# Kernel optimization log

Measured on AMD Instinct MI355X. Metric: run time of the kernel, lower is better.

The kernel has to match this reference:

```python
import jax, jax.numpy as jnp
import numpy as np

N = 131072

def _project(feat, x, y):
    # bilinear sample: feat is [H, W, C], x/y are float pixel coords [N]
    x1 = jnp.floor(x); x2 = jnp.ceil(x)
    y1 = jnp.floor(y); y2 = jnp.ceil(y)
    xi1 = x1.astype(jnp.int32); xi2 = x2.astype(jnp.int32)
    yi1 = y1.astype(jnp.int32); yi2 = y2.astype(jnp.int32)
    # JAX clamps out-of-range gather indices (matches GPU tf.gather_nd edge behavior)
    Q11 = feat[xi1, yi1]
    Q12 = feat[xi1, yi2]
    Q21 = feat[xi2, yi1]
    Q22 = feat[xi2, yi2]
    w11 = ((x2 - x) * (y2 - y))[:, None]
    w21 = ((x - x1) * (y2 - y))[:, None]
    w12 = ((x2 - x) * (y - y1))[:, None]
    w22 = ((x - x1) * (y - y1))[:, None]
    return w11 * Q11 + w21 * Q21 + w12 * Q12 + w22 * Q22


def setup_inputs() -> dict:
    key = jax.random.key(0)
    k1, k2, k3, k4, k5 = jax.random.split(key, 5)
    coord = jax.random.normal(k1, (N, 3), dtype=jnp.float32)
    # ensure points are in front of the camera (Z < 0) as assumed by the projection
    coord = coord.at[:, 2].set(-jnp.abs(coord[:, 2]) - 1.0)
    feat1 = jax.random.normal(k2, (56, 56, 64), dtype=jnp.float32)
    feat2 = jax.random.normal(k3, (28, 28, 128), dtype=jnp.float32)
    feat3 = jax.random.normal(k4, (14, 14, 256), dtype=jnp.float32)
    feat4 = jax.random.normal(k5, (7, 7, 512), dtype=jnp.float32)
    return {"coord": coord, "feat1": feat1, "feat2": feat2, "feat3": feat3, "feat4": feat4}


def reference(coord, feat1, feat2, feat3, feat4):
    X = coord[:, 0]; Y = coord[:, 1]; Z = coord[:, 2]
    h = 248.0 * (-Y / -Z) + 112.0
    w = 248.0 * (X / -Z) + 112.0
    h = jnp.clip(h, 0.0, 223.0)
    w = jnp.clip(w, 0.0, 223.0)
    out1 = _project(feat1, h / (224.0 / 56), w / (224.0 / 56))
    out2 = _project(feat2, h / (224.0 / 28), w / (224.0 / 28))
    out3 = _project(feat3, h / (224.0 / 14), w / (224.0 / 14))
    out4 = _project(feat4, h / (224.0 / 7), w / (224.0 / 7))
    return jnp.concatenate([coord, out1, out2, out3, out4], axis=1)
```

## Files before the change

kernel.cpp:

```cpp
#include <hip/hip_runtime.h>


typedef float f4 __attribute__((ext_vector_type(4)));
typedef f4 uf4 __attribute__((aligned(4)));

struct BL {
    f4  wt;
    int b11, b21, b12, b22;
};

template <int C, int G>
__device__ __forceinline__ BL make_bl(float x, float y) {
    float x1 = floorf(x), x2 = ceilf(x);
    float y1 = floorf(y), y2 = ceilf(y);
    int xi1 = min((int)x1, G - 1), xi2 = min((int)x2, G - 1);
    int yi1 = min((int)y1, G - 1), yi2 = min((int)y2, G - 1);
    float wx2 = x2 - x, wx1 = x - x1;
    float wy2 = y2 - y, wy1 = y - y1;
    BL r;
    r.wt = (f4){wx2 * wy2, wx1 * wy2, wx2 * wy1, wx1 * wy1};
    const int W = C / 4;
    r.b11 = (xi1 * G + yi1) * W;
    r.b21 = (xi2 * G + yi1) * W;
    r.b12 = (xi1 * G + yi2) * W;
    r.b22 = (xi2 * G + yi2) * W;
    return r;
}

__device__ __forceinline__ f4 blend(const f4* __restrict__ f, const BL& b, int cc) {
    f4 q11 = f[b.b11 + cc];
    f4 q21 = f[b.b21 + cc];
    f4 q12 = f[b.b12 + cc];
    f4 q22 = f[b.b22 + cc];
    return b.wt.x * q11 + b.wt.y * q21 + b.wt.z * q12 + b.wt.w * q22;
}

__device__ __forceinline__ void proj_hw(const float* __restrict__ coord, int p,
                                        float& h, float& w) {
    float X = coord[3 * p + 0];
    float Y = coord[3 * p + 1];
    float Z = coord[3 * p + 2];
    float hh = 248.0f * (Y / Z) + 112.0f;
    float ww = 248.0f * (X / (-Z)) + 112.0f;
    h = fminf(fmaxf(hh, 0.0f), 223.0f);
    w = fminf(fmaxf(ww, 0.0f), 223.0f);
}

__global__ void __launch_bounds__(256)
graph_projection_v2(const float* __restrict__ coord,
                    const f4* __restrict__ f1, const f4* __restrict__ f2,
                    const f4* __restrict__ f3, const f4* __restrict__ f4p,
                    float* __restrict__ out, int n) {
    const int lane = threadIdx.x & 63;
    const int wid  = (blockIdx.x * blockDim.x + threadIdx.x) >> 6;
    const int nw   = (gridDim.x * blockDim.x) >> 6;
    const int ngrp = n >> 2;

    for (int g = wid; g < ngrp; g += nw) {
        const int q = g * 4;
        float h[4], w[4];
#pragma unroll
        for (int j = 0; j < 4; ++j) proj_hw(coord, q + j, h[j], w[j]);

        if (lane < 12) {
            int j = lane / 3, k = lane - 3 * j;
            __builtin_nontemporal_store(coord[3 * q + lane],
                                        out + (size_t)963 * (q + j) + k);
        }

        {
            float hj = (lane & 32) ? ((lane & 16) ? h[3] : h[2])
                                   : ((lane & 16) ? h[1] : h[0]);
            float wj = (lane & 32) ? ((lane & 16) ? w[3] : w[2])
                                   : ((lane & 16) ? w[1] : w[0]);
            BL b = make_bl<64, 56>(hj * 0.25f, wj * 0.25f);
            f4 v = blend(f1, b, lane & 15);
            int j = lane >> 4;
            __builtin_nontemporal_store(
                v, (uf4*)(out + (size_t)963 * (q + j) + 3 + 4 * (lane & 15)));
        }

#pragma unroll
        for (int jj = 0; jj < 2; ++jj) {
            float hj = (lane & 32) ? h[2 * jj + 1] : h[2 * jj];
            float wj = (lane & 32) ? w[2 * jj + 1] : w[2 * jj];
            BL b = make_bl<128, 28>(hj * 0.125f, wj * 0.125f);
            f4 v = blend(f2, b, lane & 31);
            int j = 2 * jj + (lane >> 5);
            __builtin_nontemporal_store(
                v, (uf4*)(out + (size_t)963 * (q + j) + 67 + 4 * (lane & 31)));
        }

#pragma unroll
        for (int j = 0; j < 4; ++j) {
            BL b = make_bl<256, 14>(h[j] * 0.0625f, w[j] * 0.0625f);
            f4 v = blend(f3, b, lane);
            __builtin_nontemporal_store(
                v, (uf4*)(out + (size_t)963 * (q + j) + 195 + 4 * lane));
        }

#pragma unroll
        for (int j = 0; j < 4; ++j) {
            BL b = make_bl<512, 7>(h[j] * 0.03125f, w[j] * 0.03125f);
            f4 v0 = blend(f4p, b, lane);
            f4 v1 = blend(f4p, b, lane + 64);
            float* base = out + (size_t)963 * (q + j) + 451;
            __builtin_nontemporal_store(v0, (uf4*)(base + 4 * lane));
            __builtin_nontemporal_store(v1, (uf4*)(base + 256 + 4 * lane));
        }
    }

    for (int p = (n & ~3) + wid; p < n; p += nw) {
        float h0, w0;
        proj_hw(coord, p, h0, w0);
        if (lane < 3) out[(size_t)963 * p + lane] = coord[3 * p + lane];
        {
            BL b = make_bl<64, 56>(h0 * 0.25f, w0 * 0.25f);
            if (lane < 16) {
                f4 v = blend(f1, b, lane);
                *(uf4*)(out + (size_t)963 * p + 3 + 4 * lane) = v;
            }
        }
        {
            BL b = make_bl<128, 28>(h0 * 0.125f, w0 * 0.125f);
            if (lane < 32) {
                f4 v = blend(f2, b, lane);
                *(uf4*)(out + (size_t)963 * p + 67 + 4 * lane) = v;
            }
        }
        {
            BL b = make_bl<256, 14>(h0 * 0.0625f, w0 * 0.0625f);
            f4 v = blend(f3, b, lane);
            *(uf4*)(out + (size_t)963 * p + 195 + 4 * lane) = v;
        }
        {
            BL b = make_bl<512, 7>(h0 * 0.03125f, w0 * 0.03125f);
            f4 v0 = blend(f4p, b, lane);
            f4 v1 = blend(f4p, b, lane + 64);
            *(uf4*)(out + (size_t)963 * p + 451 + 4 * lane) = v0;
            *(uf4*)(out + (size_t)963 * p + 451 + 256 + 4 * lane) = v1;
        }
    }
}

extern "C" void kernel_launch(void* const* d_in, const int* in_sizes, int n_in,
                              void* d_out, int out_size, void* d_ws, size_t ws_size,
                              hipStream_t stream) {
    const float* coord = (const float*)d_in[0];
    const f4* f1 = (const f4*)d_in[1];
    const f4* f2 = (const f4*)d_in[2];
    const f4* f3 = (const f4*)d_in[3];
    const f4* f4p = (const f4*)d_in[4];
    float* out = (float*)d_out;

    const int n = in_sizes[0] / 3;

    dim3 block(256);
    dim3 grid(2048);
    graph_projection_v2<<<grid, block, 0, stream>>>(coord, f1, f2, f3, f4p, out, n);
}
```

Before: 582.9 us.

## Stage per-wave output rows in LDS and write back with aligned vector stores

After: 541.5 us. -7.1%, faster.

```diff
diff --git a/kernel.cpp b/kernel.cpp
--- a/kernel.cpp
+++ b/kernel.cpp
@@ -46,12 +46,22 @@
     w = fminf(fmaxf(ww, 0.0f), 223.0f);
 }
 
+__device__ __forceinline__ void lds_put4(float* __restrict__ p, f4 v) {
+    p[0] = v.x; p[1] = v.y; p[2] = v.z; p[3] = v.w;
+}
+
+#define WAVE_LDS 3856
+
 __global__ void __launch_bounds__(256)
-graph_projection_v2(const float* __restrict__ coord,
+graph_projection_v3(const float* __restrict__ coord,
                     const f4* __restrict__ f1, const f4* __restrict__ f2,
                     const f4* __restrict__ f3, const f4* __restrict__ f4p,
                     float* __restrict__ out, int n) {
+    __shared__ __align__(16) float lds[4 * WAVE_LDS];
     const int lane = threadIdx.x & 63;
+    const int wv   = threadIdx.x >> 6;
+    float* __restrict__ lb = lds + wv * WAVE_LDS;
+
     const int wid  = (blockIdx.x * blockDim.x + threadIdx.x) >> 6;
     const int nw   = (gridDim.x * blockDim.x) >> 6;
     const int ngrp = n >> 2;
@@ -64,8 +74,7 @@
 
         if (lane < 12) {
             int j = lane / 3, k = lane - 3 * j;
-            __builtin_nontemporal_store(coord[3 * q + lane],
-                                        out + (size_t)963 * (q + j) + k);
+            lb[j * 963 + k] = coord[3 * q + lane];
         }
 
         {
@@ -76,8 +85,7 @@
             BL b = make_bl<64, 56>(hj * 0.25f, wj * 0.25f);
             f4 v = blend(f1, b, lane & 15);
             int j = lane >> 4;
-            __builtin_nontemporal_store(
-                v, (uf4*)(out + (size_t)963 * (q + j) + 3 + 4 * (lane & 15)));
+            lds_put4(lb + j * 963 + 3 + 4 * (lane & 15), v);
         }
 
 #pragma unroll
@@ -87,16 +95,14 @@
             BL b = make_bl<128, 28>(hj * 0.125f, wj * 0.125f);
             f4 v = blend(f2, b, lane & 31);
             int j = 2 * jj + (lane >> 5);
-            __builtin_nontemporal_store(
-                v, (uf4*)(out + (size_t)963 * (q + j) + 67 + 4 * (lane & 31)));
+            lds_put4(lb + j * 963 + 67 + 4 * (lane & 31), v);
         }
 
 #pragma unroll
         for (int j = 0; j < 4; ++j) {
             BL b = make_bl<256, 14>(h[j] * 0.0625f, w[j] * 0.0625f);
             f4 v = blend(f3, b, lane);
-            __builtin_nontemporal_store(
-                v, (uf4*)(out + (size_t)963 * (q + j) + 195 + 4 * lane));
+            lds_put4(lb + j * 963 + 195 + 4 * lane, v);
         }
 
 #pragma unroll
@@ -104,10 +110,17 @@
             BL b = make_bl<512, 7>(h[j] * 0.03125f, w[j] * 0.03125f);
             f4 v0 = blend(f4p, b, lane);
             f4 v1 = blend(f4p, b, lane + 64);
-            float* base = out + (size_t)963 * (q + j) + 451;
-            __builtin_nontemporal_store(v0, (uf4*)(base + 4 * lane));
-            __builtin_nontemporal_store(v1, (uf4*)(base + 256 + 4 * lane));
+            lds_put4(lb + j * 963 + 451 + 4 * lane, v0);
+            lds_put4(lb + j * 963 + 451 + 256 + 4 * lane, v1);
         }
+
+        const f4* __restrict__ lv = (const f4*)lb;
+        f4* __restrict__ gb = (f4*)(out + (size_t)3852 * g);
+#pragma unroll
+        for (int k = 0; k < 15; ++k)
+            __builtin_nontemporal_store(lv[(k << 6) + lane], gb + (k << 6) + lane);
+        if (lane < 3)
+            __builtin_nontemporal_store(lv[960 + lane], gb + 960 + lane);
     }
 
     for (int p = (n & ~3) + wid; p < n; p += nw) {
@@ -157,5 +170,5 @@
 
     dim3 block(256);
     dim3 grid(2048);
-    graph_projection_v2<<<grid, block, 0, stream>>>(coord, f1, f2, f3, f4p, out, n);
+    graph_projection_v3<<<grid, block, 0, stream>>>(coord, f1, f2, f3, f4p, out, n);
 }
```

## Stage per-wave output rows in LDS to emit aligned contiguous 16-byte stores

Applied to the files above, without the earlier changes.

New measurement: 524.8 us. 10.0% less time.

```diff
diff --git a/kernel.cpp b/kernel.cpp
--- a/kernel.cpp
+++ b/kernel.cpp
@@ -3,6 +3,11 @@
 
 typedef float f4 __attribute__((ext_vector_type(4)));
 typedef f4 uf4 __attribute__((aligned(4)));
+
+#define LDS_FENCE() do { \
+    asm volatile("" ::: "memory"); \
+    __builtin_amdgcn_sched_barrier(0); \
+} while (0)
 
 struct BL {
     f4  wt;
@@ -46,68 +51,126 @@
     w = fminf(fmaxf(ww, 0.0f), 223.0f);
 }
 
-__global__ void __launch_bounds__(256)
-graph_projection_v2(const float* __restrict__ coord,
+__device__ __forceinline__ void compute_phase(float* __restrict__ lb,
+                                              const float* __restrict__ coord,
+                                              const f4* __restrict__ f1,
+                                              const f4* __restrict__ f2,
+                                              const f4* __restrict__ f3,
+                                              const f4* __restrict__ f4p,
+                                              int p0, int lane) {
+    float h0, w0, h1, w1;
+    proj_hw(coord, p0,     h0, w0);
+    proj_hw(coord, p0 + 1, h1, w1);
+
+    if (lane < 6) {
+        int j = lane / 3, k = lane - 3 * j;
+        lb[j * 964 + k] = coord[3 * p0 + lane];
+    }
+
+    if (lane < 32) {
+        int j = (lane >> 4) & 1;
+        float hj = (lane & 16) ? h1 : h0;
+        float wj = (lane & 16) ? w1 : w0;
+        BL b = make_bl<64, 56>(hj * 0.25f, wj * 0.25f);
+        f4 v = blend(f1, b, lane & 15);
+        *(f4*)(lb + j * 964 + 4 + 4 * (lane & 15)) = v;
+    }
+    {
+        int j = lane >> 5;
+        float hj = (lane & 32) ? h1 : h0;
+        float wj = (lane & 32) ? w1 : w0;
+        BL b = make_bl<128, 28>(hj * 0.125f, wj * 0.125f);
+        f4 v = blend(f2, b, lane & 31);
+        *(f4*)(lb + j * 964 + 68 + 4 * (lane & 31)) = v;
+    }
+#pragma unroll
+    for (int j = 0; j < 2; ++j) {
+        float hj = j ? h1 : h0, wj = j ? w1 : w0;
+        BL b = make_bl<256, 14>(hj * 0.0625f, wj * 0.0625f);
+        f4 v = blend(f3, b, lane);
+        *(f4*)(lb + j * 964 + 196 + 4 * lane) = v;
+    }
+#pragma unroll
+    for (int j = 0; j < 2; ++j) {
+        float hj = j ? h1 : h0, wj = j ? w1 : w0;
+        BL b = make_bl<512, 7>(hj * 0.03125f, wj * 0.03125f);
+        f4 v0 = blend(f4p, b, lane);
+        f4 v1 = blend(f4p, b, lane + 64);
+        *(f4*)(lb + j * 964 + 452 + 4 * lane) = v0;
+        *(f4*)(lb + j * 964 + 452 + 256 + 4 * lane) = v1;
+    }
+}
+
+__device__ __forceinline__ float lread(const float* __restrict__ lb, int m) {
+    int j = (m >= 963) ? 1 : 0;
+    int k = m - 963 * j;
+    return lb[m + j + (k >= 3 ? 1 : 0)];
+}
+
+__global__ void __launch_bounds__(256, 5)
+graph_projection_v5(const float* __restrict__ coord,
                     const f4* __restrict__ f1, const f4* __restrict__ f2,
                     const f4* __restrict__ f3, const f4* __restrict__ f4p,
                     float* __restrict__ out, int n) {
+    __shared__ __align__(16) float lds[4][1928];
     const int lane = threadIdx.x & 63;
+    const int wv   = threadIdx.x >> 6;
+    float* __restrict__ lb = lds[wv];
+
     const int wid  = (blockIdx.x * blockDim.x + threadIdx.x) >> 6;
     const int nw   = (gridDim.x * blockDim.x) >> 6;
     const int ngrp = n >> 2;
 
     for (int g = wid; g < ngrp; g += nw) {
-        const int q = g * 4;
-        float h[4], w[4];
-#pragma unroll
-        for (int j = 0; j < 4; ++j) proj_hw(coord, q + j, h[j], w[j]);
-
-        if (lane < 12) {
-            int j = lane / 3, k = lane - 3 * j;
-            __builtin_nontemporal_store(coord[3 * q + lane],
-                                        out + (size_t)963 * (q + j) + k);
-        }
-
-        {
-            float hj = (lane & 32) ? ((lane & 16) ? h[3] : h[2])
-                                   : ((lane & 16) ? h[1] : h[0]);
-            float wj = (lane & 32) ? ((lane & 16) ? w[3] : w[2])
-                                   : ((lane & 16) ? w[1] : w[0]);
-            BL b = make_bl<64, 56>(hj * 0.25f, wj * 0.25f);
-            f4 v = blend(f1, b, lane & 15);
-            int j = lane >> 4;
-            __builtin_nontemporal_store(
-                v, (uf4*)(out + (size_t)963 * (q + j) + 3 + 4 * (lane & 15)));
-        }
-
-#pragma unroll
-        for (int jj = 0; jj < 2; ++jj) {
-            float hj = (lane & 32) ? h[2 * jj + 1] : h[2 * jj];
-            float wj = (lane & 32) ? w[2 * jj + 1] : w[2 * jj];
-            BL b = make_bl<128, 28>(hj * 0.125f, wj * 0.125f);
-            f4 v = blend(f2, b, lane & 31);
-            int j = 2 * jj + (lane >> 5);
-            __builtin_nontemporal_store(
-                v, (uf4*)(out + (size_t)963 * (q + j) + 67 + 4 * (lane & 31)));
-        }
-
-#pragma unroll
-        for (int j = 0; j < 4; ++j) {
-            BL b = make_bl<256, 14>(h[j] * 0.0625f, w[j] * 0.0625f);
-            f4 v = blend(f3, b, lane);
-            __builtin_nontemporal_store(
-                v, (uf4*)(out + (size_t)963 * (q + j) + 195 + 4 * lane));
-        }
-
-#pragma unroll
-        for (int j = 0; j < 4; ++j) {
-            BL b = make_bl<512, 7>(h[j] * 0.03125f, w[j] * 0.03125f);
-            f4 v0 = blend(f4p, b, lane);
-            f4 v1 = blend(f4p, b, lane + 64);
-            float* base = out + (size_t)963 * (q + j) + 451;
-            __builtin_nontemporal_store(v0, (uf4*)(base + 4 * lane));
-            __builtin_nontemporal_store(v1, (uf4*)(base + 256 + 4 * lane));
-        }
+        const int q = 4 * g;
+        f4* __restrict__ gb = (f4*)(out + (size_t)3852 * g);
+
+        compute_phase(lb, coord, f1, f2, f3, f4p, q, lane);
+        LDS_FENCE();
+        {
+            const float c2x = coord[3 * (q + 2) + 0];
+            const float c2y = coord[3 * (q + 2) + 1];
+#pragma unroll
+            for (int kk = 0; kk < 7; ++kk) {
+                int fi = (kk << 6) + lane;
+                int m0 = fi * 4;
+                f4 v = {lread(lb, m0), lread(lb, m0 + 1),
+                        lread(lb, m0 + 2), lread(lb, m0 + 3)};
+                __builtin_nontemporal_store(v, gb + fi);
+            }
+            if (lane < 34) {
+                int fi = 448 + lane;
+                int m0 = fi * 4;
+                f4 v;
+                v.x = lread(lb, m0);
+                v.y = lread(lb, m0 + 1);
+                if (fi == 481) { v.z = c2x; v.w = c2y; }
+                else { v.z = lread(lb, m0 + 2); v.w = lread(lb, m0 + 3); }
+                __builtin_nontemporal_store(v, gb + fi);
+            }
+        }
+        LDS_FENCE();
+
+        compute_phase(lb, coord, f1, f2, f3, f4p, q + 2, lane);
+        LDS_FENCE();
+        {
+#pragma unroll
+            for (int kk = 0; kk < 7; ++kk) {
+                int fi = 482 + (kk << 6) + lane;
+                int m0 = fi * 4 - 1926;
+                f4 v = {lread(lb, m0), lread(lb, m0 + 1),
+                        lread(lb, m0 + 2), lread(lb, m0 + 3)};
+                __builtin_nontemporal_store(v, gb + fi);
+            }
+            if (lane < 33) {
+                int fi = 930 + lane;
+                int m0 = fi * 4 - 1926;
+                f4 v = {lread(lb, m0), lread(lb, m0 + 1),
+                        lread(lb, m0 + 2), lread(lb, m0 + 3)};
+                __builtin_nontemporal_store(v, gb + fi);
+            }
+        }
+        LDS_FENCE();
     }
 
     for (int p = (n & ~3) + wid; p < n; p += nw) {
@@ -157,5 +220,5 @@
 
     dim3 block(256);
     dim3 grid(2048);
-    graph_projection_v2<<<grid, block, 0, stream>>>(coord, f1, f2, f3, f4p, out, n);
-}
+    graph_projection_v5<<<grid, block, 0, stream>>>(coord, f1, f2, f3, f4p, out, n);
+}
```
